# Kernel tuning notes

Hardware: AMD Instinct MI355X
Metric: run time of the kernel (lower is better)

## Reference

```python
import jax, jax.numpy as jnp
import numpy as np

B, CTX, EMBED, VOCAB = 4096, 20, 100, 50000


def setup_inputs() -> dict:
    key = jax.random.key(0)
    k1, k2, k3, k4, k5, k6 = jax.random.split(key, 6)
    context = jax.random.randint(k1, (B, CTX), 0, VOCAB)
    mu_lambda = jax.random.normal(k2, (B, EMBED), dtype=jnp.float32)
    sigma_lambda = jax.random.uniform(k3, (B, EMBED), dtype=jnp.float32) + 0.5  # strictly positive
    mu_x = jax.random.normal(k4, (B, EMBED), dtype=jnp.float32)
    sigma_x = jax.random.uniform(k5, (B, EMBED), dtype=jnp.float32) + 0.5
    decoded = jax.random.uniform(k6, (B, VOCAB), dtype=jnp.float32) + 1e-3  # positive probs
    return {"context": context, "mu_lambda": mu_lambda, "sigma_lambda": sigma_lambda,
            "mu_x": mu_x, "sigma_x": sigma_x, "decoded": decoded}


def reference(context, mu_lambda, sigma_lambda, mu_x, sigma_x, decoded):
    # log-likelihood: sum over context words of log decoded[word_id]  -> [B]
    gathered = jnp.take_along_axis(decoded, context, axis=1)  # [B, CTX]
    ll = jnp.sum(jnp.log(gathered), axis=1)
    # diagonal-Gaussian KL(q(lambda) || p(x)) summed over embed dims -> [B]
    kl = jnp.sum(
        jnp.log(sigma_x / sigma_lambda)
        + (sigma_lambda ** 2 + (mu_lambda - mu_x) ** 2) / (2.0 * sigma_x ** 2)
        - 0.5,
        axis=1,
    )
    return -ll + kl  # [B] per-example negative ELBO
```

## Files before the change

kernel.cpp:

```cpp
#include <hip/hip_runtime.h>


constexpr int B_     = 4096;
constexpr int CTX_   = 20;
constexpr int EMBED_ = 100;
constexpr int VOCAB_ = 50000;

__global__ __launch_bounds__(256) void elbo_kernel(
    const int*   __restrict__ context,
    const float* __restrict__ mu_lambda,
    const float* __restrict__ sigma_lambda,
    const float* __restrict__ mu_x,
    const float* __restrict__ sigma_x,
    const float* __restrict__ decoded,
    float*       __restrict__ out)
{
    const int wave = (int)((blockIdx.x * blockDim.x + threadIdx.x) >> 6);
    const int lane = (int)(threadIdx.x & 63);
    if (wave >= B_) return;

    const float* mul = mu_lambda    + (size_t)wave * EMBED_;
    const float* sl  = sigma_lambda + (size_t)wave * EMBED_;
    const float* mux = mu_x         + (size_t)wave * EMBED_;
    const float* sx  = sigma_x      + (size_t)wave * EMBED_;

    float acc = 0.0f;

    {
        int e = lane;
        float s_l = sl[e], s_x = sx[e];
        float dmu = mul[e] - mux[e];
        acc += __logf(s_x) - __logf(s_l)
             + (s_l * s_l + dmu * dmu) / (2.0f * s_x * s_x) - 0.5f;
    }
    if (lane + 64 < EMBED_) {
        int e = lane + 64;
        float s_l = sl[e], s_x = sx[e];
        float dmu = mul[e] - mux[e];
        acc += __logf(s_x) - __logf(s_l)
             + (s_l * s_l + dmu * dmu) / (2.0f * s_x * s_x) - 0.5f;
    }

    if (lane < CTX_) {
        int idx = context[(size_t)wave * CTX_ + lane];
        float g = decoded[(size_t)wave * VOCAB_ + idx];
        acc -= __logf(g);
    }

    #pragma unroll
    for (int off = 32; off > 0; off >>= 1)
        acc += __shfl_xor(acc, off, 64);

    if (lane == 0) out[wave] = acc;
}

extern "C" void kernel_launch(void* const* d_in, const int* in_sizes, int n_in,
                              void* d_out, int out_size, void* d_ws, size_t ws_size,
                              hipStream_t stream) {
    const int*   context      = (const int*)  d_in[0];
    const float* mu_lambda    = (const float*)d_in[1];
    const float* sigma_lambda = (const float*)d_in[2];
    const float* mu_x         = (const float*)d_in[3];
    const float* sigma_x      = (const float*)d_in[4];
    const float* decoded      = (const float*)d_in[5];
    float* out = (float*)d_out;

    const int threads = 256;
    const int blocks  = (B_ * 64) / threads;
    elbo_kernel<<<blocks, threads, 0, stream>>>(
        context, mu_lambda, sigma_lambda, mu_x, sigma_x, decoded, out);
}
```

Baseline: 9.360 us.

## Split each example across two waves and combine halves via shared memory

Each example is now handled by two wavefronts, each covering half of the embedding dims and half of the context gathers, so a block of 256 threads processes two examples and the grid doubles. The context index load is issued early so the dependent gather can start sooner, and the KL term uses fast reciprocals and a single log instead of divisions and two logs. The two wave partials are summed through shared memory after a block barrier. The aim is to shorten per-wave latency on the dependent gather chain. The cost is a sync, more blocks and slightly less precise arithmetic.

```diff
diff --git a/kernel.cpp b/kernel.cpp
--- a/kernel.cpp
+++ b/kernel.cpp
@@ -15,35 +15,34 @@
     const float* __restrict__ decoded,
     float*       __restrict__ out)
 {
-    const int wave = (int)((blockIdx.x * blockDim.x + threadIdx.x) >> 6);
-    const int lane = (int)(threadIdx.x & 63);
-    if (wave >= B_) return;
+    __shared__ float partial[4];
 
-    const float* mul = mu_lambda    + (size_t)wave * EMBED_;
-    const float* sl  = sigma_lambda + (size_t)wave * EMBED_;
-    const float* mux = mu_x         + (size_t)wave * EMBED_;
-    const float* sx  = sigma_x      + (size_t)wave * EMBED_;
+    const int tid  = (int)threadIdx.x;
+    const int w    = tid >> 6;
+    const int lane = tid & 63;
+    const int exL  = w >> 1;
+    const int half = w & 1;
+    const int b    = (int)blockIdx.x * 2 + exL;
+
+    int idx = 0;
+    const bool do_gather = (lane < CTX_ / 2);
+    if (do_gather)
+        idx = context[(size_t)b * CTX_ + half * (CTX_ / 2) + lane];
 
     float acc = 0.0f;
 
-    {
-        int e = lane;
-        float s_l = sl[e], s_x = sx[e];
-        float dmu = mul[e] - mux[e];
-        acc += __logf(s_x) - __logf(s_l)
-             + (s_l * s_l + dmu * dmu) / (2.0f * s_x * s_x) - 0.5f;
-    }
-    if (lane + 64 < EMBED_) {
-        int e = lane + 64;
-        float s_l = sl[e], s_x = sx[e];
-        float dmu = mul[e] - mux[e];
-        acc += __logf(s_x) - __logf(s_l)
-             + (s_l * s_l + dmu * dmu) / (2.0f * s_x * s_x) - 0.5f;
+    if (lane < EMBED_ / 2) {
+        const size_t eb = (size_t)b * EMBED_ + half * (EMBED_ / 2) + lane;
+        float s_l = sigma_lambda[eb];
+        float s_x = sigma_x[eb];
+        float dmu = mu_lambda[eb] - mu_x[eb];
+        float inv = __fdividef(1.0f, s_x);
+        acc = __logf(s_x * __fdividef(1.0f, s_l))
+            + (s_l * s_l + dmu * dmu) * 0.5f * inv * inv - 0.5f;
     }
 
-    if (lane < CTX_) {
-        int idx = context[(size_t)wave * CTX_ + lane];
-        float g = decoded[(size_t)wave * VOCAB_ + idx];
+    if (do_gather) {
+        float g = decoded[(size_t)b * VOCAB_ + idx];
         acc -= __logf(g);
     }
 
@@ -51,7 +50,11 @@
     for (int off = 32; off > 0; off >>= 1)
         acc += __shfl_xor(acc, off, 64);
 
-    if (lane == 0) out[wave] = acc;
+    if (lane == 0) partial[w] = acc;
+    __syncthreads();
+
+    if (tid < 2)
+        out[(size_t)blockIdx.x * 2 + tid] = partial[2 * tid] + partial[2 * tid + 1];
 }
 
 extern "C" void kernel_launch(void* const* d_in, const int* in_sizes, int n_in,
@@ -66,7 +69,7 @@
     float* out = (float*)d_out;
 
     const int threads = 256;
-    const int blocks  = (B_ * 64) / threads;
+    const int blocks  = B_ / 2;
     elbo_kernel<<<blocks, threads, 0, stream>>>(
         context, mu_lambda, sigma_lambda, mu_x, sigma_x, decoded, out);
 }
```

Measured after the change: 9.695 us. +3.6%, slower.
